# Optimization experiments

Hardware: AMD Instinct MI355X
Metric: run time of the kernel (lower is better)

## Reference

```python
import jax, jax.numpy as jnp
import numpy as np

B, S, E, H, V = 1024, 64, 100, 512, 50000


def _gru_backward_last(x, wih, whh, bih, bhh):
    # x: [B,S,E]; PyTorch GRU cell, reverse direction; return final hidden [B,H]
    def step(h, xt):
        gi = xt @ wih.T + bih          # [B,3H]
        gh = h @ whh.T + bhh           # [B,3H]
        ir, iz, i_n = jnp.split(gi, 3, axis=-1)
        hr, hz, h_n = jnp.split(gh, 3, axis=-1)
        r = jax.nn.sigmoid(ir + hr)
        z = jax.nn.sigmoid(iz + hz)
        n = jnp.tanh(i_n + r * h_n)
        return (1.0 - z) * n + z * h, None
    h0 = jnp.zeros((x.shape[0], whh.shape[1]), x.dtype)
    hT, _ = jax.lax.scan(step, h0, x.transpose(1, 0, 2), reverse=True)
    return hT


def _encode(tokens, emb, wih, whh, bih, bhh):
    return _gru_backward_last(emb[tokens], wih, whh, bih, bhh)


def setup_inputs() -> dict:
    key = jax.random.key(0)
    ks = jax.random.split(key, 32)
    d = {}
    d['query'] = jax.random.randint(ks[0], (B, S), 0, V)
    d['context'] = jax.random.randint(ks[1], (B, S), 0, V)
    d['reply'] = jax.random.randint(ks[2], (B, S), 0, V)
    i = 3
    for tag in ('q', 'c', 'r'):
        d[f'emb_{tag}'] = jax.random.uniform(ks[i], (V, E), jnp.float32, -0.25, 0.25); i += 1
        d[f'wih_{tag}'] = jax.random.normal(ks[i], (3 * H, E), jnp.float32) * 0.05; i += 1
        d[f'whh_{tag}'] = jax.random.normal(ks[i], (3 * H, H), jnp.float32) * 0.05; i += 1
        d[f'bih_{tag}'] = jnp.zeros((3 * H,), jnp.float32); i += 1
        d[f'bhh_{tag}'] = jnp.zeros((3 * H,), jnp.float32); i += 1
    d['lin_w'] = jax.random.normal(ks[i], (H, H), jnp.float32) * 0.02
    d['lin_b'] = jnp.zeros((H,), jnp.float32)
    return d


def reference(query, context, reply,
              emb_q, wih_q, whh_q, bih_q, bhh_q,
              emb_c, wih_c, whh_c, bih_c, bhh_c,
              emb_r, wih_r, whh_r, bih_r, bhh_r,
              lin_w, lin_b):
    eq = _encode(query, emb_q, wih_q, whh_q, bih_q, bhh_q)    # [B,H]
    ec = _encode(context, emb_c, wih_c, whh_c, bih_c, bhh_c)  # [B,H]
    er = _encode(reply, emb_r, wih_r, whh_r, bih_r, bhh_r)    # [B,H]
    eqc = ((eq + ec) * 0.5) @ lin_w.T + lin_b                  # [B,H]
    sim = lambda a: jax.nn.softmax(a @ er.T, axis=-1)          # [B,B]
    return sim(eq), sim(ec), sim(eqc)
```

## Files before the change

### kernel.cpp

```cpp
#include <hip/hip_runtime.h>

typedef unsigned short u16;
typedef __attribute__((ext_vector_type(8))) short short8;
typedef __attribute__((ext_vector_type(4))) float f32x4;

#define B_   1024
#define S_   64
#define E_   100
#define H_   512
#define G3_  1536
#define XW_  256
#define WSZG (32 * 3 * 60 * 512)
#define GS_  (60 * 512)

__device__ __forceinline__ float bf2f(u16 u) {
    union { unsigned int u; float f; } c; c.u = ((unsigned int)u) << 16; return c.f;
}
__device__ __forceinline__ u16 f2bf(float f) {
    union { float f; unsigned int u; } c; c.f = f;
    unsigned int r = c.u + 0x7fffu + ((c.u >> 16) & 1u);
    return (u16)(r >> 16);
}
__device__ __forceinline__ f32x4 mfma16(short8 a, short8 b, f32x4 c) {
    return __builtin_amdgcn_mfma_f32_16x16x32_bf16(a, b, c, 0, 0, 0);
}

__global__ __launch_bounds__(256) void gather_kernel(
    const int* __restrict__ tok, const float* __restrict__ emb, u16* __restrict__ xs)
{
    int tid = threadIdx.x;
    int hw  = tid & 31;
    int rowid = blockIdx.x * 8 + (tid >> 5);
    int t = rowid >> 10, b = rowid & 1023;
    int token = tok[b * S_ + t];
    const float* src = emb + (long)token * E_;
    u16* dst = xs + (long)rowid * XW_;
    int c0 = hw * 4;
    u16 a1[4], a2[4];
    #pragma unroll
    for (int j = 0; j < 4; ++j) {
        int c = c0 + j;
        float v = (c < E_) ? src[c] : 0.f;
        u16 h = f2bf(v);
        a1[j] = h;
        a2[j] = f2bf(v - bf2f(h));
    }
    uint2 p1, p2;
    p1.x = (unsigned)a1[0] | ((unsigned)a1[1] << 16);
    p1.y = (unsigned)a1[2] | ((unsigned)a1[3] << 16);
    p2.x = (unsigned)a2[0] | ((unsigned)a2[1] << 16);
    p2.y = (unsigned)a2[2] | ((unsigned)a2[3] << 16);
    *(uint2*)(dst + c0)       = p1;
    *(uint2*)(dst + 128 + c0) = p2;
}

__global__ __launch_bounds__(256) void repack_swz(
    const float* __restrict__ wih, const float* __restrict__ whh, u16* __restrict__ out)
{
    long idx = (long)blockIdx.x * 256 + threadIdx.x;
    int jj   = idx & 7;
    int lane = (idx >> 3) & 63;
    int q9   = (int)(idx >> 9);
    int ks   = q9 % 60;
    int q    = q9 / 60;
    int gate = q % 3;
    int ht   = q / 3;
    int n   = ht * 16 + (lane & 15);
    int k   = ks * 32 + (lane >> 4) * 8 + jj;
    int row = gate * H_ + n;
    float w; int lo;
    if (k < 384) {
        int kk = k & 127, grp = k >> 7;
        if (kk >= E_) { out[idx] = 0; return; }
        w = wih[row * E_ + kk];
        lo = (grp == 2);
    } else {
        int kh = k - 384;
        int kk = kh & 511, grp = kh >> 9;
        w = whh[row * H_ + kk];
        lo = (grp == 2);
    }
    u16 h = f2bf(w);
    if (lo) h = f2bf(w - bf2f(h));
    out[idx] = h;
}

__global__ __launch_bounds__(256) void repack_lin(
    const float* __restrict__ lw, u16* __restrict__ l1, u16* __restrict__ l2)
{
    int i = blockIdx.x * 256 + threadIdx.x;
    float w = lw[i];
    u16 h = f2bf(w);
    l1[i] = h;
    l2[i] = f2bf(w - bf2f(h));
}

struct BiasPtrs { const float* bih[3]; const float* bhh[3]; };

__global__ __launch_bounds__(256, 3) void gru_step(
    const u16* __restrict__ xs,
    const u16* __restrict__ wswz,
    BiasPtrs bp,
    const u16* __restrict__ h1_in, const u16* __restrict__ h2_in,
    u16* __restrict__ h1_out, u16* __restrict__ h2_out,
    int t)
{
    __shared__ __attribute__((aligned(16))) u16 As[2 * 64 * 72];
    const int tid = threadIdx.x;
    const int lane = tid & 63;
    const int kh = tid >> 7;
    const int nh = (tid >> 6) & 1;
    const int l15 = lane & 15, l4 = lane >> 4;
    const int htp = blockIdx.x;
    const int m0  = blockIdx.y * 64;
    const int g   = blockIdx.z;
    const int ht  = htp * 2 + nh;

    const u16* wg  = wswz + (long)g * WSZG + (long)ht * (3 * GS_) + lane * 8;
    const u16* xb  = xs + ((long)(g * S_ + t) * B_ + m0) * XW_;
    const u16* hb1 = h1_in + ((long)g * B_ + m0) * H_;
    const u16* hb2 = h2_in + ((long)g * B_ + m0) * H_;
    u16* slotp = As + kh * (64 * 72);

    f32x4 zero = {0.f, 0.f, 0.f, 0.f};
    f32x4 acc_r[4]  = {zero, zero, zero, zero};
    f32x4 acc_z[4]  = {zero, zero, zero, zero};
    f32x4 acc_ni[4] = {zero, zero, zero, zero};
    f32x4 acc_nh[4] = {zero, zero, zero, zero};

    auto stage2 = [&](const u16* s0, const u16* s1, int stride) {
        #pragma unroll
        for (int i = 0; i < 2; ++i) {
            int s = tid + 256 * i;
            int row = s >> 3, seg = s & 7;
            *(uint4*)(&As[row * 72 + seg * 8]) =
                *(const uint4*)(s0 + (long)row * stride + seg * 8);
            *(uint4*)(&As[64 * 72 + row * 72 + seg * 8]) =
                *(const uint4*)(s1 + (long)row * stride + seg * 8);
        }
    };
    auto consume_dual = [&](const u16* b1, const u16* b2, f32x4* accn) {
        #pragma unroll
        for (int ksl = 0; ksl < 2; ++ksl) {
            short8 br1 = *(const short8*)(b1 + ksl * 512);
            short8 bz1 = *(const short8*)(b1 + GS_ + ksl * 512);
            short8 bn1 = *(const short8*)(b1 + 2 * GS_ + ksl * 512);
            short8 br2 = *(const short8*)(b2 + ksl * 512);
            short8 bz2 = *(const short8*)(b2 + GS_ + ksl * 512);
            short8 bn2 = *(const short8*)(b2 + 2 * GS_ + ksl * 512);
            short8 a[4];
            #pragma unroll
            for (int q = 0; q < 4; ++q)
                a[q] = *(const short8*)(&slotp[(q * 16 + l15) * 72 + ksl * 32 + l4 * 8]);
            #pragma unroll
            for (int q = 0; q < 4; ++q) {
                acc_r[q] = mfma16(a[q], br1, acc_r[q]);
                acc_z[q] = mfma16(a[q], bz1, acc_z[q]);
                accn[q]  = mfma16(a[q], bn1, accn[q]);
                acc_r[q] = mfma16(a[q], br2, acc_r[q]);
                acc_z[q] = mfma16(a[q], bz2, acc_z[q]);
                accn[q]  = mfma16(a[q], bn2, accn[q]);
            }
        }
    };
    auto consume_single = [&](const u16* b1, f32x4* accn) {
        #pragma unroll
        for (int ksl = 0; ksl < 2; ++ksl) {
            short8 br1 = *(const short8*)(b1 + ksl * 512);
            short8 bz1 = *(const short8*)(b1 + GS_ + ksl * 512);
            short8 bn1 = *(const short8*)(b1 + 2 * GS_ + ksl * 512);
            short8 a[4];
            #pragma unroll
            for (int q = 0; q < 4; ++q)
                a[q] = *(const short8*)(&slotp[(q * 16 + l15) * 72 + ksl * 32 + l4 * 8]);
            #pragma unroll
            for (int q = 0; q < 4; ++q) {
                acc_r[q] = mfma16(a[q], br1, acc_r[q]);
                acc_z[q] = mfma16(a[q], bz1, acc_z[q]);
                accn[q]  = mfma16(a[q], bn1, accn[q]);
            }
        }
    };

    stage2(xb, xb + 64, XW_);
    __syncthreads();
    consume_dual(wg + (2 * kh) * 512, wg + (8 + 2 * kh) * 512, acc_ni);
    __syncthreads();
    stage2(xb + 128, xb + 192, XW_);
    __syncthreads();
    consume_single(wg + (4 + 2 * kh) * 512, acc_ni);
    __syncthreads();
    #pragma unroll 1
    for (int i = 0; i < 4; ++i) {
        stage2(hb1 + i * 64, hb1 + (i + 4) * 64, H_);
        __syncthreads();
        consume_dual(wg + (12 + 8 * kh + 2 * i) * 512,
                     wg + (44 + 8 * kh + 2 * i) * 512, acc_nh);
        __syncthreads();
    }
    #pragma unroll 1
    for (int i = 0; i < 4; ++i) {
        stage2(hb2 + i * 64, hb2 + (i + 4) * 64, H_);
        __syncthreads();
        consume_single(wg + (28 + 8 * kh + 2 * i) * 512, acc_nh);
        __syncthreads();
    }

    f32x4* rp = (f32x4*)As;
    const int ridx = (nh * 64 + lane) * 8;
    if (kh == 1) {
        #pragma unroll
        for (int q = 0; q < 4; ++q) { rp[ridx + q] = acc_r[q]; rp[ridx + 4 + q] = acc_z[q]; }
    }
    __syncthreads();
    if (kh == 0) {
        #pragma unroll
        for (int q = 0; q < 4; ++q) { acc_r[q] += rp[ridx + q]; acc_z[q] += rp[ridx + 4 + q]; }
    }
    __syncthreads();
    if (kh == 1) {
        #pragma unroll
        for (int q = 0; q < 4; ++q) { rp[ridx + q] = acc_ni[q]; rp[ridx + 4 + q] = acc_nh[q]; }
    }
    __syncthreads();
    if (kh == 0) {
        #pragma unroll
        for (int q = 0; q < 4; ++q) { acc_ni[q] += rp[ridx + q]; acc_nh[q] += rp[ridx + 4 + q]; }

        int hc = ht * 16 + l15;
        const float* bih = bp.bih[g];
        const float* bhh = bp.bhh[g];
        float b_ir = bih[hc],          b_hr = bhh[hc];
        float b_iz = bih[H_ + hc],     b_hz = bhh[H_ + hc];
        float b_in = bih[2 * H_ + hc], b_hn = bhh[2 * H_ + hc];
        #pragma unroll
        for (int mt = 0; mt < 4; ++mt) {
            #pragma unroll
            for (int i = 0; i < 4; ++i) {
                int m = m0 + mt * 16 + l4 * 4 + i;
                long idx = ((long)g * B_ + m) * H_ + hc;
                float pr = acc_r[mt][i] + b_ir + b_hr;
                float pz = acc_z[mt][i] + b_iz + b_hz;
                float vi = acc_ni[mt][i] + b_in;
                float vh = acc_nh[mt][i] + b_hn;
                float r = 1.f / (1.f + __expf(-pr));
                float z = 1.f / (1.f + __expf(-pz));
                float n = tanhf(vi + r * vh);
                float hold = bf2f(h1_in[idx]) + bf2f(h2_in[idx]);
                float hnew = (1.f - z) * n + z * hold;
                u16 hh = f2bf(hnew);
                h1_out[idx] = hh;
                h2_out[idx] = f2bf(hnew - bf2f(hh));
            }
        }
    }
}

__global__ __launch_bounds__(256) void qc_kernel(
    const u16* __restrict__ h1, const u16* __restrict__ h2,
    u16* __restrict__ q1, u16* __restrict__ q2)
{
    int i = blockIdx.x * 256 + threadIdx.x;
    float eq = bf2f(h1[i]) + bf2f(h2[i]);
    float ec = bf2f(h1[B_ * H_ + i]) + bf2f(h2[B_ * H_ + i]);
    float q = 0.5f * (eq + ec);
    u16 h = f2bf(q);
    q1[i] = h;
    q2[i] = f2bf(q - bf2f(h));
}

struct GArgs { const u16* a[24]; const u16* b[24]; };

__global__ __launch_bounds__(256) void gemm_nt(
    GArgs ga, int nch, int astr, int bstr,
    const float* __restrict__ bias, float* __restrict__ outf,
    u16* __restrict__ ohi, u16* __restrict__ olo, int ldc, int mode)
{
    __shared__ __attribute__((aligned(16))) u16 As[64 * 72];
    __shared__ __attribute__((aligned(16))) u16 Bs[64 * 72];
    const int tid = threadIdx.x;
    const int w = tid >> 6, lane = tid & 63;
    const int l15 = lane & 15, l4 = lane >> 4;
    const int m0 = blockIdx.x * 64, n0 = blockIdx.y * 64;

    f32x4 zero = {0.f, 0.f, 0.f, 0.f};
    f32x4 acc[4] = {zero, zero, zero, zero};

    for (int c = 0; c < nch; ++c) {
        int row = tid >> 2, seg = tid & 3;
        const u16* sa = ga.a[c] + (long)(m0 + row) * astr + seg * 16;
        *(uint4*)(&As[row * 72 + seg * 16])     = *(const uint4*)(sa);
        *(uint4*)(&As[row * 72 + seg * 16 + 8]) = *(const uint4*)(sa + 8);
        const u16* sb = ga.b[c] + (long)(n0 + row) * bstr + seg * 16;
        *(uint4*)(&Bs[row * 72 + seg * 16])     = *(const uint4*)(sb);
        *(uint4*)(&Bs[row * 72 + seg * 16 + 8]) = *(const uint4*)(sb + 8);
        __syncthreads();
        #pragma unroll
        for (int ks = 0; ks < 2; ++ks) {
            short8 bfrag = *(const short8*)(&Bs[(w * 16 + l15) * 72 + ks * 32 + l4 * 8]);
            #pragma unroll
            for (int rt = 0; rt < 4; ++rt) {
                short8 a = *(const short8*)(&As[(rt * 16 + l15) * 72 + ks * 32 + l4 * 8]);
                acc[rt] = mfma16(a, bfrag, acc[rt]);
            }
        }
        __syncthreads();
    }

    int n = n0 + w * 16 + l15;
    float bv = bias ? bias[n] : 0.f;
    #pragma unroll
    for (int rt = 0; rt < 4; ++rt) {
        #pragma unroll
        for (int i = 0; i < 4; ++i) {
            int m = m0 + rt * 16 + l4 * 4 + i;
            float v = acc[rt][i] + bv;
            if (mode == 0) {
                outf[(long)m * ldc + n] = v;
            } else {
                u16 h = f2bf(v);
                ohi[(long)m * ldc + n] = h;
                olo[(long)m * ldc + n] = f2bf(v - bf2f(h));
            }
        }
    }
}

__global__ __launch_bounds__(256) void softmax_kernel(
    const float* __restrict__ lg, float* __restrict__ out)
{
    __shared__ float red[256];
    int row = blockIdx.x, tid = threadIdx.x;
    const float* src = lg + (long)row * 1024;
    float x[4];
    float mx = -1e30f;
    #pragma unroll
    for (int i = 0; i < 4; ++i) { x[i] = src[tid + 256 * i]; mx = fmaxf(mx, x[i]); }
    red[tid] = mx; __syncthreads();
    for (int s = 128; s > 0; s >>= 1) { if (tid < s) red[tid] = fmaxf(red[tid], red[tid + s]); __syncthreads(); }
    mx = red[0]; __syncthreads();
    float sm = 0.f;
    #pragma unroll
    for (int i = 0; i < 4; ++i) { x[i] = __expf(x[i] - mx); sm += x[i]; }
    red[tid] = sm; __syncthreads();
    for (int s = 128; s > 0; s >>= 1) { if (tid < s) red[tid] += red[tid + s]; __syncthreads(); }
    float inv = 1.f / red[0];
    float* dst = out + (long)row * 1024;
    #pragma unroll
    for (int i = 0; i < 4; ++i) dst[tid + 256 * i] = x[i] * inv;
}

extern "C" void kernel_launch(void* const* d_in, const int* in_sizes, int n_in,
                              void* d_out, int out_size, void* d_ws, size_t ws_size,
                              hipStream_t stream)
{
    const int* tok[3] = {(const int*)d_in[0], (const int*)d_in[1], (const int*)d_in[2]};
    const float *emb[3], *wih[3], *whh[3], *bih[3], *bhh[3];
    for (int g = 0; g < 3; ++g) {
        emb[g] = (const float*)d_in[3 + 5 * g];
        wih[g] = (const float*)d_in[4 + 5 * g];
        whh[g] = (const float*)d_in[5 + 5 * g];
        bih[g] = (const float*)d_in[6 + 5 * g];
        bhh[g] = (const float*)d_in[7 + 5 * g];
    }
    const float* lin_w = (const float*)d_in[18];
    const float* lin_b = (const float*)d_in[19];

    char* ws = (char*)d_ws;
    size_t off = 0;
    auto alloc = [&](size_t bytes) { void* p = ws + off; off += (bytes + 255) & ~255ull; return p; };

    const size_t BH  = (size_t)B_ * H_;
    const size_t PRB = 3 * BH * 2;
    const size_t PING = 2 * PRB;

    u16*   Xs   = (u16*)alloc(3ll * S_ * B_ * XW_ * 2);
    u16*   Wswz = (u16*)alloc(3ll * WSZG * 2);
    u16*   LW1  = (u16*)alloc((size_t)H_ * H_ * 2);
    u16*   LW2  = (u16*)alloc((size_t)H_ * H_ * 2);
    char*  HB   = (char*)alloc(2 * PING);
    u16*   QC1  = (u16*)alloc(BH * 2);
    u16*   QC2  = (u16*)alloc(BH * 2);
    u16*   EQ1  = (u16*)alloc(BH * 2);
    u16*   EQ2  = (u16*)alloc(BH * 2);
    float* LG   = (float*)alloc(3ll * B_ * B_ * 4);

    u16* H1[2]; u16* H2[2];
    for (int i = 0; i < 2; ++i) {
        char* pb = HB + (size_t)i * PING;
        H1[i] = (u16*)pb;
        H2[i] = (u16*)(pb + PRB);
    }

    hipMemsetAsync(HB, 0, PING, stream);

    for (int g = 0; g < 3; ++g) {
        gather_kernel<<<dim3(S_ * B_ / 8), 256, 0, stream>>>(tok[g], emb[g], Xs + (size_t)g * S_ * B_ * XW_);
        repack_swz<<<dim3(WSZG / 256), 256, 0, stream>>>(wih[g], whh[g], Wswz + (size_t)g * WSZG);
    }
    repack_lin<<<dim3(H_ * H_ / 256), 256, 0, stream>>>(lin_w, LW1, LW2);

    BiasPtrs bp;
    for (int g = 0; g < 3; ++g) { bp.bih[g] = bih[g]; bp.bhh[g] = bhh[g]; }

    int p = 0;
    for (int t = S_ - 1; t >= 0; --t) {
        gru_step<<<dim3(16, 16, 3), 256, 0, stream>>>(Xs, Wswz, bp,
            H1[p], H2[p], H1[1 - p], H2[1 - p], t);
        p ^= 1;
    }
    const u16* H1F = H1[p];
    const u16* H2F = H2[p];

    qc_kernel<<<dim3(BH / 256), 256, 0, stream>>>(H1F, H2F, QC1, QC2);

    GArgs ga;
    for (int c = 0; c < 8; ++c)   { ga.a[c] = QC1 + c * 64;        ga.b[c] = LW1 + c * 64; }
    for (int c = 8; c < 16; ++c)  { ga.a[c] = QC2 + (c - 8) * 64;  ga.b[c] = LW1 + (c - 8) * 64; }
    for (int c = 16; c < 24; ++c) { ga.a[c] = QC1 + (c - 16) * 64; ga.b[c] = LW2 + (c - 16) * 64; }
    gemm_nt<<<dim3(16, 8), 256, 0, stream>>>(ga, 24, H_, H_, lin_b, nullptr, EQ1, EQ2, H_, 1);

    const u16* R1 = H1F + 2 * BH;
    const u16* R2 = H2F + 2 * BH;
    for (int g = 0; g < 3; ++g) {
        const u16 *A1, *A2;
        if (g == 0)      { A1 = H1F;      A2 = H2F; }
        else if (g == 1) { A1 = H1F + BH; A2 = H2F + BH; }
        else             { A1 = EQ1;      A2 = EQ2; }
        GArgs gs;
        for (int c = 0; c < 8; ++c)   { gs.a[c] = A1 + c * 64;        gs.b[c] = R1 + c * 64; }
        for (int c = 8; c < 16; ++c)  { gs.a[c] = A2 + (c - 8) * 64;  gs.b[c] = R1 + (c - 8) * 64; }
        for (int c = 16; c < 24; ++c) { gs.a[c] = A1 + (c - 16) * 64; gs.b[c] = R2 + (c - 16) * 64; }
        gemm_nt<<<dim3(16, 16), 256, 0, stream>>>(gs, 24, H_, H_, nullptr,
            LG + (size_t)g * B_ * B_, nullptr, nullptr, B_, 0);
    }

    softmax_kernel<<<dim3(3 * B_), 256, 0, stream>>>(LG, (float*)d_out);
}
```

Measured before the change: 2.301 ms.

## Double-buffer LDS staging with register prefetch in GRU step kernel

```diff
diff --git a/kernel.cpp b/kernel.cpp
--- a/kernel.cpp
+++ b/kernel.cpp
@@ -105,7 +105,7 @@
     u16* __restrict__ h1_out, u16* __restrict__ h2_out,
     int t)
 {
-    __shared__ __attribute__((aligned(16))) u16 As[2 * 64 * 72];
+    __shared__ __attribute__((aligned(16))) u16 As[2][2][64 * 72];
     const int tid = threadIdx.x;
     const int lane = tid & 63;
     const int kh = tid >> 7;
@@ -120,7 +120,6 @@
     const u16* xb  = xs + ((long)(g * S_ + t) * B_ + m0) * XW_;
     const u16* hb1 = h1_in + ((long)g * B_ + m0) * H_;
     const u16* hb2 = h2_in + ((long)g * B_ + m0) * H_;
-    u16* slotp = As + kh * (64 * 72);
 
     f32x4 zero = {0.f, 0.f, 0.f, 0.f};
     f32x4 acc_r[4]  = {zero, zero, zero, zero};
@@ -128,18 +127,26 @@
     f32x4 acc_ni[4] = {zero, zero, zero, zero};
     f32x4 acc_nh[4] = {zero, zero, zero, zero};
 
-    auto stage2 = [&](const u16* s0, const u16* s1, int stride) {
+    uint4 r[4];
+    auto load2 = [&](const u16* s0, const u16* s1, int stride) {
         #pragma unroll
         for (int i = 0; i < 2; ++i) {
             int s = tid + 256 * i;
             int row = s >> 3, seg = s & 7;
-            *(uint4*)(&As[row * 72 + seg * 8]) =
-                *(const uint4*)(s0 + (long)row * stride + seg * 8);
-            *(uint4*)(&As[64 * 72 + row * 72 + seg * 8]) =
-                *(const uint4*)(s1 + (long)row * stride + seg * 8);
+            r[2 * i]     = *(const uint4*)(s0 + (long)row * stride + seg * 8);
+            r[2 * i + 1] = *(const uint4*)(s1 + (long)row * stride + seg * 8);
         }
     };
-    auto consume_dual = [&](const u16* b1, const u16* b2, f32x4* accn) {
+    auto write2 = [&](int buf) {
+        #pragma unroll
+        for (int i = 0; i < 2; ++i) {
+            int s = tid + 256 * i;
+            int row = s >> 3, seg = s & 7;
+            *(uint4*)(&As[buf][0][row * 72 + seg * 8]) = r[2 * i];
+            *(uint4*)(&As[buf][1][row * 72 + seg * 8]) = r[2 * i + 1];
+        }
+    };
+    auto consume_dual = [&](const u16* sp, const u16* b1, const u16* b2, f32x4* accn) {
         #pragma unroll
         for (int ksl = 0; ksl < 2; ++ksl) {
             short8 br1 = *(const short8*)(b1 + ksl * 512);
@@ -151,7 +158,7 @@
             short8 a[4];
             #pragma unroll
             for (int q = 0; q < 4; ++q)
-                a[q] = *(const short8*)(&slotp[(q * 16 + l15) * 72 + ksl * 32 + l4 * 8]);
+                a[q] = *(const short8*)(&sp[(q * 16 + l15) * 72 + ksl * 32 + l4 * 8]);
             #pragma unroll
             for (int q = 0; q < 4; ++q) {
                 acc_r[q] = mfma16(a[q], br1, acc_r[q]);
@@ -163,7 +170,7 @@
             }
         }
     };
-    auto consume_single = [&](const u16* b1, f32x4* accn) {
+    auto consume_single = [&](const u16* sp, const u16* b1, f32x4* accn) {
         #pragma unroll
         for (int ksl = 0; ksl < 2; ++ksl) {
             short8 br1 = *(const short8*)(b1 + ksl * 512);
@@ -172,7 +179,7 @@
             short8 a[4];
             #pragma unroll
             for (int q = 0; q < 4; ++q)
-                a[q] = *(const short8*)(&slotp[(q * 16 + l15) * 72 + ksl * 32 + l4 * 8]);
+                a[q] = *(const short8*)(&sp[(q * 16 + l15) * 72 + ksl * 32 + l4 * 8]);
             #pragma unroll
             for (int q = 0; q < 4; ++q) {
                 acc_r[q] = mfma16(a[q], br1, acc_r[q]);
@@ -182,29 +189,47 @@
         }
     };
 
-    stage2(xb, xb + 64, XW_);
-    __syncthreads();
-    consume_dual(wg + (2 * kh) * 512, wg + (8 + 2 * kh) * 512, acc_ni);
-    __syncthreads();
-    stage2(xb + 128, xb + 192, XW_);
-    __syncthreads();
-    consume_single(wg + (4 + 2 * kh) * 512, acc_ni);
-    __syncthreads();
-    #pragma unroll 1
-    for (int i = 0; i < 4; ++i) {
-        stage2(hb1 + i * 64, hb1 + (i + 4) * 64, H_);
-        __syncthreads();
-        consume_dual(wg + (12 + 8 * kh + 2 * i) * 512,
-                     wg + (44 + 8 * kh + 2 * i) * 512, acc_nh);
-        __syncthreads();
-    }
-    #pragma unroll 1
-    for (int i = 0; i < 4; ++i) {
-        stage2(hb2 + i * 64, hb2 + (i + 4) * 64, H_);
-        __syncthreads();
-        consume_single(wg + (28 + 8 * kh + 2 * i) * 512, acc_nh);
-        __syncthreads();
-    }
+    load2(xb, xb + 64, XW_);
+    write2(0);
+
+    __syncthreads();
+    load2(xb + 128, xb + 192, XW_);
+    consume_dual(&As[0][kh][0], wg + (2 * kh) * 512, wg + (8 + 2 * kh) * 512, acc_ni);
+    write2(1);
+    __syncthreads();
+    load2(hb1, hb1 + 4 * 64, H_);
+    consume_single(&As[1][kh][0], wg + (4 + 2 * kh) * 512, acc_ni);
+    write2(0);
+    __syncthreads();
+    load2(hb1 + 64, hb1 + 5 * 64, H_);
+    consume_dual(&As[0][kh][0], wg + (12 + 8 * kh) * 512, wg + (44 + 8 * kh) * 512, acc_nh);
+    write2(1);
+    __syncthreads();
+    load2(hb1 + 2 * 64, hb1 + 6 * 64, H_);
+    consume_dual(&As[1][kh][0], wg + (12 + 8 * kh + 2) * 512, wg + (44 + 8 * kh + 2) * 512, acc_nh);
+    write2(0);
+    __syncthreads();
+    load2(hb1 + 3 * 64, hb1 + 7 * 64, H_);
+    consume_dual(&As[0][kh][0], wg + (12 + 8 * kh + 4) * 512, wg + (44 + 8 * kh + 4) * 512, acc_nh);
+    write2(1);
+    __syncthreads();
+    load2(hb2, hb2 + 4 * 64, H_);
+    consume_dual(&As[1][kh][0], wg + (12 + 8 * kh + 6) * 512, wg + (44 + 8 * kh + 6) * 512, acc_nh);
+    write2(0);
+    __syncthreads();
+    load2(hb2 + 64, hb2 + 5 * 64, H_);
+    consume_single(&As[0][kh][0], wg + (28 + 8 * kh) * 512, acc_nh);
+    write2(1);
+    __syncthreads();
+    load2(hb2 + 2 * 64, hb2 + 6 * 64, H_);
+    consume_single(&As[1][kh][0], wg + (28 + 8 * kh + 2) * 512, acc_nh);
+    write2(0);
+    __syncthreads();
+    load2(hb2 + 3 * 64, hb2 + 7 * 64, H_);
+    consume_single(&As[0][kh][0], wg + (28 + 8 * kh + 4) * 512, acc_nh);
+    write2(1);
+    __syncthreads();
+    consume_single(&As[1][kh][0], wg + (28 + 8 * kh + 6) * 512, acc_nh);
 
     f32x4* rp = (f32x4*)As;
     const int ridx = (nh * 64 + lane) * 8;
```

After: 3.393 ms. 1.47x slower.
